# Kernel optimization log

Measured on AMD Instinct MI355X. Metric: run time of the kernel, lower is better.

## Reference

```python
import jax, jax.numpy as jnp
import numpy as np

D = 512      # model_dim
H = 8        # num_heads
HD = D // H  # head_dim = 64
S = 196      # tokens per channel (14x14 grid)
CHANNELS = np.array([2, 4, 6, 4], dtype=np.int32)  # multiplex channels per sample


def setup_inputs() -> dict:
    key = jax.random.key(0)
    ks = jax.random.split(key, 8)
    C = int(CHANNELS.sum())  # 16
    n = lambda k, shp, s=1.0: jax.random.normal(k, shp, dtype=jnp.float32) * s
    return {
        "x_query": n(ks[0], (C, S, D)),
        "x_keyval": n(ks[1], (C, S, D)),
        "pos": n(ks[2], (C, S, D)),
        "channels": CHANNELS,
        "Wq": n(ks[3], (D, D), 0.02), "bq": jnp.zeros((D,), jnp.float32),
        "Wk": n(ks[4], (D, D), 0.02), "bk": jnp.zeros((D,), jnp.float32),
        "Wv": n(ks[5], (D, D), 0.02), "bv": jnp.zeros((D,), jnp.float32),
        "Wo": n(ks[6], (D, D), 0.02), "bo": jnp.zeros((D,), jnp.float32),
    }


def reference(x_query, x_keyval, pos, channels, Wq, bq, Wk, bk, Wv, bv, Wo, bo):
    C, S_, D_ = x_query.shape
    ch = np.asarray(channels)
    # segment id per packed token; segment i has length channels[i]*S (== cu_seq_len blocks)
    seg = np.repeat(np.arange(ch.shape[0]), ch * S_)                # [T] static
    block_mask = seg[:, None] == seg[None, :]                        # [T,T] static bool

    xq = x_query.reshape(-1, D_)   # [T,D]
    xk = x_keyval.reshape(-1, D_)
    p = pos.reshape(-1, D_)

    # positional embedding fused into Q/K before projection (query_pos/key_pos)
    q = ((xq + p) @ Wq + bq).reshape(-1, H, HD)
    k = ((xk + p) @ Wk + bk).reshape(-1, H, HD)
    v = (xk @ Wv + bv).reshape(-1, H, HD)

    scale = 1.0 / np.sqrt(HD)
    scores = jnp.einsum('qhd,khd->hqk', q, k) * scale               # [H,T,T]
    scores = jnp.where(block_mask[None], scores, jnp.float32(-1e30))
    attn = jax.nn.softmax(scores, axis=-1)
    out = jnp.einsum('hqk,khd->qhd', attn, v).reshape(-1, D_)       # [T,D]
    out = out @ Wo + bo
    return out.reshape(C, S_, D_)
```

## Files before the change

kernel.cpp:

```cpp
#include <hip/hip_runtime.h>
#include <hip/hip_bf16.h>


typedef short short8 __attribute__((ext_vector_type(8)));
typedef float f32x4 __attribute__((ext_vector_type(4)));

__device__ __forceinline__ float b2f(unsigned short u) {
    union { float f; unsigned int i; } x; x.i = ((unsigned int)u) << 16; return x.f;
}
__device__ __forceinline__ unsigned short f2b(float f) {
    union { float f; unsigned int i; } x; x.f = f;
    unsigned int r = x.i + 0x7fffu + ((x.i >> 16) & 1u);
    return (unsigned short)(r >> 16);
}

#define NE 1605632
#define WE 262144
#define GS 72

__launch_bounds__(256)
__global__ void prep(const float* __restrict__ W0, const float* __restrict__ W1,
                     const float* __restrict__ W2, const float* __restrict__ W3,
                     unsigned short* __restrict__ WF) {
    const int tid = threadIdx.x;
    const float* W = blockIdx.z == 0 ? W0 : blockIdx.z == 1 ? W1 : blockIdx.z == 2 ? W2 : W3;
    unsigned short* T = WF + (size_t)blockIdx.z * WE;
    const int s = blockIdx.x * 4 + (tid >> 6);
    const int f = s >> 4, t = s & 15;
    const int lane = tid & 63, quad = lane >> 4, l16 = lane & 15;
    short8 o;
    #pragma unroll
    for (int j = 0; j < 8; ++j)
        o[j] = (short)f2b(W[(size_t)(t * 32 + quad * 8 + j) * 512 + f * 16 + l16]);
    *(short8*)(T + (size_t)s * 512 + lane * 8) = o;
}

__device__ __forceinline__ short8 castA(const float* __restrict__ X,
                                        const float* __restrict__ P, size_t off) {
    f32x4 x0 = *(const f32x4*)(X + off), x1 = *(const f32x4*)(X + off + 4);
    short8 r;
    if (P) {
        f32x4 p0 = *(const f32x4*)(P + off), p1 = *(const f32x4*)(P + off + 4);
        #pragma unroll
        for (int j = 0; j < 4; ++j) {
            r[j] = (short)f2b(x0[j] + p0[j]); r[4 + j] = (short)f2b(x1[j] + p1[j]);
        }
    } else {
        #pragma unroll
        for (int j = 0; j < 4; ++j) {
            r[j] = (short)f2b(x0[j]); r[4 + j] = (short)f2b(x1[j]);
        }
    }
    return r;
}

template <bool OUT_F32>
__device__ __forceinline__ void gemm_wave(const unsigned short* __restrict__ A,
                                          const unsigned short* __restrict__ WFw,
                                          const float* __restrict__ bias,
                                          void* __restrict__ C,
                                          int m0, int n0) {
    const int lane = threadIdx.x & 63;
    const int quad = lane >> 4, l16 = lane & 15;
    const int f0 = n0 >> 4;
    const unsigned short* Arow = A + (size_t)(m0 + l16) * 512 + quad * 8;
    const unsigned short* Bbase = WFw + (size_t)lane * 8;

    f32x4 acc[4] = {};
    #pragma unroll 4
    for (int t = 0; t < 16; ++t) {
        short8 af = *(const short8*)(Arow + t * 32);
        #pragma unroll
        for (int nt = 0; nt < 4; ++nt) {
            short8 bf = *(const short8*)(Bbase + (size_t)((f0 + nt) * 16 + t) * 512);
            acc[nt] = __builtin_amdgcn_mfma_f32_16x16x32_bf16(af, bf, acc[nt], 0, 0, 0);
        }
    }
    #pragma unroll
    for (int nt = 0; nt < 4; ++nt) {
        const int col = n0 + nt * 16 + l16;
        const float bv = bias[col];
        #pragma unroll
        for (int r = 0; r < 4; ++r) {
            const int row = m0 + quad * 4 + r;
            float cv = acc[nt][r] + bv;
            if constexpr (OUT_F32) ((float*)C)[(size_t)row * 512 + col] = cv;
            else ((unsigned short*)C)[(size_t)row * 512 + col] = f2b(cv);
        }
    }
}

__device__ __forceinline__ void gemm_wave32c(const float* __restrict__ X,
                                             const float* __restrict__ P,
                                             const unsigned short* __restrict__ WFw,
                                             const float* __restrict__ bias,
                                             unsigned short* __restrict__ C,
                                             int m0, int n0) {
    const int lane = threadIdx.x & 63;
    const int quad = lane >> 4, l16 = lane & 15;
    const int f0 = n0 >> 4;
    const size_t a0 = (size_t)(m0 + l16) * 512 + quad * 8;
    const unsigned short* Bbase = WFw + (size_t)lane * 8;

    f32x4 acc0[4] = {}, acc1[4] = {};
    #pragma unroll 4
    for (int t = 0; t < 16; ++t) {
        short8 af0 = castA(X, P, a0 + t * 32);
        short8 af1 = castA(X, P, a0 + 16 * 512 + t * 32);
        #pragma unroll
        for (int nt = 0; nt < 4; ++nt) {
            short8 bf = *(const short8*)(Bbase + (size_t)((f0 + nt) * 16 + t) * 512);
            acc0[nt] = __builtin_amdgcn_mfma_f32_16x16x32_bf16(af0, bf, acc0[nt], 0, 0, 0);
            acc1[nt] = __builtin_amdgcn_mfma_f32_16x16x32_bf16(af1, bf, acc1[nt], 0, 0, 0);
        }
    }
    #pragma unroll
    for (int nt = 0; nt < 4; ++nt) {
        const int col = n0 + nt * 16 + l16;
        const float bv = bias[col];
        #pragma unroll
        for (int r = 0; r < 4; ++r) {
            const int row = m0 + quad * 4 + r;
            C[(size_t)row * 512 + col]        = f2b(acc0[nt][r] + bv);
            C[(size_t)(row + 16) * 512 + col] = f2b(acc1[nt][r] + bv);
        }
    }
}

__launch_bounds__(256)
__global__ void qkv_gemm(const float* __restrict__ xq, const float* __restrict__ xk,
                         const float* __restrict__ pos,
                         const unsigned short* __restrict__ WF,
                         const float* __restrict__ bq, const float* __restrict__ bk,
                         const float* __restrict__ bv,
                         unsigned short* __restrict__ qb, unsigned short* __restrict__ kb,
                         unsigned short* __restrict__ vb) {
    const float* X; const float* P; const unsigned short* WFw; const float* bias;
    unsigned short* C;
    switch (blockIdx.z) {
        case 0:  X = xq; P = pos;     WFw = WF;          bias = bq; C = qb; break;
        case 1:  X = xk; P = pos;     WFw = WF + WE;     bias = bk; C = kb; break;
        default: X = xk; P = nullptr; WFw = WF + 2 * WE; bias = bv; C = vb; break;
    }
    const int w = threadIdx.x >> 6;
    gemm_wave32c(X, P, WFw, bias, C, blockIdx.x * 64 + (w & 1) * 32,
                 blockIdx.y * 128 + (w >> 1) * 64);
}

__launch_bounds__(256)
__global__ void out_gemm(const unsigned short* __restrict__ A,
                         const unsigned short* __restrict__ WFo,
                         const float* __restrict__ bo, float* __restrict__ out) {
    gemm_wave<true>(A, WFo, bo, out, blockIdx.x * 64 + (threadIdx.x >> 6) * 16,
                    blockIdx.y * 64);
}

__launch_bounds__(512)
__global__ void attn_seg(const unsigned short* __restrict__ q,
                         const unsigned short* __restrict__ k,
                         const unsigned short* __restrict__ v,
                         unsigned short* __restrict__ o) {
    __shared__ __align__(16) unsigned char Lds[55296];

    const int id = blockIdx.x;
    int h, off, L, qt;
    if (id < 152)      { h = id & 7; qt = id >> 3; off = 1176; L = 1176; }
    else if (id < 360) { int m = id - 152; h = m & 7; int s = m >> 3;
                         if (s < 13) { off = 392;  L = 784; qt = s; }
                         else        { off = 2352; L = 784; qt = s - 13; } }
    else               { int m = id - 360; h = m & 7; qt = m >> 3; off = 0; L = 392; }

    const int tid = threadIdx.x;
    const int wave = tid >> 6, lane = tid & 63;
    const int grp = wave >> 2, w4 = wave & 3;
    const int quad = lane >> 4, l16 = lane & 15;
    const int hb = h * 64;
    const int lastr = off + L - 1;

    unsigned short* Ks = (unsigned short*)(Lds + grp * 18432);
    unsigned short* Vt = (unsigned short*)(Lds + grp * 18432 + 9216);
    unsigned char*  Pme = Lds + 36864 + wave * 2304;

    int qrow = off + qt * 64 + w4 * 16 + l16;
    if (qrow > lastr) qrow = lastr;
    const short8 qf0 = *(const short8*)(q + (size_t)qrow * 512 + hb + quad * 8);
    const short8 qf1 = *(const short8*)(q + (size_t)qrow * 512 + hb + 32 + quad * 8);

    const int skey = lane, sd = w4 * 16;
    const int ntiles = (L + 63) >> 6;
    const int nt0 = (ntiles + 1) >> 1;

    float lsum = 0.f;
    f32x4 oacc[4] = {};

    short8 kr0, kr1, vr0, vr1;
    {
        int kk = (grp ? nt0 : 0) * 64 + skey;
        int krow = off + (kk < L ? kk : L - 1);
        kr0 = *(const short8*)(k + (size_t)krow * 512 + hb + sd);
        kr1 = *(const short8*)(k + (size_t)krow * 512 + hb + sd + 8);
        vr0 = *(const short8*)(v + (size_t)krow * 512 + hb + sd);
        vr1 = *(const short8*)(v + (size_t)krow * 512 + hb + sd + 8);
    }
    unsigned char* pwr = Pme + l16 * 144 + quad * 8;
    const unsigned char* prd = Pme + l16 * 144 + quad * 16;

    for (int i = 0; i < nt0; ++i) {
        const int tg = (grp ? nt0 : 0) + i;
        __syncthreads();
        *(short8*)(Ks + skey * GS + sd)     = kr0;
        *(short8*)(Ks + skey * GS + sd + 8) = kr1;
        #pragma unroll
        for (int j = 0; j < 8; ++j) {
            Vt[(sd + j) * GS + skey]     = (unsigned short)vr0[j];
            Vt[(sd + 8 + j) * GS + skey] = (unsigned short)vr1[j];
        }
        __syncthreads();
        if (i + 1 < nt0) {
            int kk = (tg + 1) * 64 + skey;
            int krow = off + (kk < L ? kk : L - 1);
            kr0 = *(const short8*)(k + (size_t)krow * 512 + hb + sd);
            kr1 = *(const short8*)(k + (size_t)krow * 512 + hb + sd + 8);
            vr0 = *(const short8*)(v + (size_t)krow * 512 + hb + sd);
            vr1 = *(const short8*)(v + (size_t)krow * 512 + hb + sd + 8);
        }
        f32x4 sT[4];
        #pragma unroll
        for (int g = 0; g < 4; ++g) {
            short8 kb0 = *(const short8*)(Ks + (g * 16 + l16) * GS + quad * 8);
            short8 kb1 = *(const short8*)(Ks + (g * 16 + l16) * GS + 32 + quad * 8);
            f32x4 z = {0.f, 0.f, 0.f, 0.f};
            z     = __builtin_amdgcn_mfma_f32_16x16x32_bf16(kb0, qf0, z, 0, 0, 0);
            sT[g] = __builtin_amdgcn_mfma_f32_16x16x32_bf16(kb1, qf1, z, 0, 0, 0);
        }
        const int kbase = tg * 64 + quad * 4;
        #pragma unroll
        for (int g = 0; g < 4; ++g) {
            float p[4];
            #pragma unroll
            for (int r = 0; r < 4; ++r) {
                const bool valid = (kbase + g * 16 + r) < L;
                p[r] = valid ? __expf(fminf(sT[g][r] * 0.125f, 30.f)) : 0.f;
                lsum += p[r];
            }
            #pragma unroll
            for (int i2 = 0; i2 < 2; ++i2) {
                __hip_bfloat162 t = __float22bfloat162_rn(make_float2(p[2 * i2], p[2 * i2 + 1]));
                *(unsigned int*)(pwr + g * 32 + i2 * 4) = *(unsigned int*)&t;
            }
        }
        short8 pa0 = *(const short8*)(prd);
        short8 pa1 = *(const short8*)(prd + 64);
        #pragma unroll
        for (int nt = 0; nt < 4; ++nt) {
            short8 vf0 = *(const short8*)(Vt + (nt * 16 + l16) * GS + quad * 8);
            short8 vf1 = *(const short8*)(Vt + (nt * 16 + l16) * GS + 32 + quad * 8);
            oacc[nt] = __builtin_amdgcn_mfma_f32_16x16x32_bf16(pa0, vf0, oacc[nt], 0, 0, 0);
            oacc[nt] = __builtin_amdgcn_mfma_f32_16x16x32_bf16(pa1, vf1, oacc[nt], 0, 0, 0);
        }
    }
    lsum += __shfl_xor(lsum, 16);
    lsum += __shfl_xor(lsum, 32);

    __syncthreads();
    float* Mrg = (float*)(Lds + w4 * 5120 + lane * 80);
    float* Ls  = (float*)(Lds + 20480);
    if (grp == 1) {
        #pragma unroll
        for (int nt = 0; nt < 4; ++nt) *(f32x4*)(Mrg + nt * 4) = oacc[nt];
        Ls[w4 * 64 + lane] = lsum;
    }
    __syncthreads();
    if (grp == 0) {
        lsum += Ls[w4 * 64 + lane];
        #pragma unroll
        for (int nt = 0; nt < 4; ++nt) {
            f32x4 po = *(const f32x4*)(Mrg + nt * 4);
            oacc[nt] += po;
        }
        #pragma unroll
        for (int r = 0; r < 4; ++r) {
            const float srow = __shfl(lsum, (lane & 48) + quad * 4 + r);
            const float linv = 1.0f / srow;
            const int qi = qt * 64 + w4 * 16 + quad * 4 + r;
            if (qi < L) {
                #pragma unroll
                for (int nt = 0; nt < 4; ++nt)
                    o[(size_t)(off + qi) * 512 + hb + nt * 16 + l16] = f2b(oacc[nt][r] * linv);
            }
        }
    }
}

extern "C" void kernel_launch(void* const* d_in, const int* in_sizes, int n_in,
                              void* d_out, int out_size, void* d_ws, size_t ws_size,
                              hipStream_t stream) {
    const float* xq  = (const float*)d_in[0];
    const float* xk  = (const float*)d_in[1];
    const float* pos = (const float*)d_in[2];
    const float* Wq = (const float*)d_in[4];
    const float* bq = (const float*)d_in[5];
    const float* Wk = (const float*)d_in[6];
    const float* bk = (const float*)d_in[7];
    const float* Wv = (const float*)d_in[8];
    const float* bv = (const float*)d_in[9];
    const float* Wo = (const float*)d_in[10];
    const float* bo = (const float*)d_in[11];
    float* out = (float*)d_out;

    unsigned short* ws = (unsigned short*)d_ws;
    unsigned short* qb = ws;
    unsigned short* kb = ws + NE;
    unsigned short* vb = ws + (size_t)2 * NE;
    unsigned short* WF = ws + (size_t)3 * NE;

    prep<<<dim3(128, 1, 4), 256, 0, stream>>>(Wq, Wk, Wv, Wo, WF);
    qkv_gemm<<<dim3(49, 4, 3), 256, 0, stream>>>(xq, xk, pos, WF, bq, bk, bv,
                                                 qb, kb, vb);
    attn_seg<<<dim3(416), 512, 0, stream>>>(qb, kb, vb, qb);
    out_gemm<<<dim3(49, 8), 256, 0, stream>>>(qb, WF + (size_t)3 * WE, bo, out);
}
```

Baseline: 165.5 us.

## Stage converted A tile in LDS and widen QKV GEMM to full N per block

```diff
diff --git a/kernel.cpp b/kernel.cpp
--- a/kernel.cpp
+++ b/kernel.cpp
@@ -5,9 +5,6 @@
 typedef short short8 __attribute__((ext_vector_type(8)));
 typedef float f32x4 __attribute__((ext_vector_type(4)));
 
-__device__ __forceinline__ float b2f(unsigned short u) {
-    union { float f; unsigned int i; } x; x.i = ((unsigned int)u) << 16; return x.f;
-}
 __device__ __forceinline__ unsigned short f2b(float f) {
     union { float f; unsigned int i; } x; x.f = f;
     unsigned int r = x.i + 0x7fffu + ((x.i >> 16) & 1u);
@@ -17,6 +14,7 @@
 #define NE 1605632
 #define WE 262144
 #define GS 72
+#define LDA 520
 
 __launch_bounds__(256)
 __global__ void prep(const float* __restrict__ W0, const float* __restrict__ W1,
@@ -35,98 +33,6 @@
     *(short8*)(T + (size_t)s * 512 + lane * 8) = o;
 }
 
-__device__ __forceinline__ short8 castA(const float* __restrict__ X,
-                                        const float* __restrict__ P, size_t off) {
-    f32x4 x0 = *(const f32x4*)(X + off), x1 = *(const f32x4*)(X + off + 4);
-    short8 r;
-    if (P) {
-        f32x4 p0 = *(const f32x4*)(P + off), p1 = *(const f32x4*)(P + off + 4);
-        #pragma unroll
-        for (int j = 0; j < 4; ++j) {
-            r[j] = (short)f2b(x0[j] + p0[j]); r[4 + j] = (short)f2b(x1[j] + p1[j]);
-        }
-    } else {
-        #pragma unroll
-        for (int j = 0; j < 4; ++j) {
-            r[j] = (short)f2b(x0[j]); r[4 + j] = (short)f2b(x1[j]);
-        }
-    }
-    return r;
-}
-
-template <bool OUT_F32>
-__device__ __forceinline__ void gemm_wave(const unsigned short* __restrict__ A,
-                                          const unsigned short* __restrict__ WFw,
-                                          const float* __restrict__ bias,
-                                          void* __restrict__ C,
-                                          int m0, int n0) {
-    const int lane = threadIdx.x & 63;
-    const int quad = lane >> 4, l16 = lane & 15;
-    const int f0 = n0 >> 4;
-    const unsigned short* Arow = A + (size_t)(m0 + l16) * 512 + quad * 8;
-    const unsigned short* Bbase = WFw + (size_t)lane * 8;
-
-    f32x4 acc[4] = {};
-    #pragma unroll 4
-    for (int t = 0; t < 16; ++t) {
-        short8 af = *(const short8*)(Arow + t * 32);
-        #pragma unroll
-        for (int nt = 0; nt < 4; ++nt) {
-            short8 bf = *(const short8*)(Bbase + (size_t)((f0 + nt) * 16 + t) * 512);
-            acc[nt] = __builtin_amdgcn_mfma_f32_16x16x32_bf16(af, bf, acc[nt], 0, 0, 0);
-        }
-    }
-    #pragma unroll
-    for (int nt = 0; nt < 4; ++nt) {
-        const int col = n0 + nt * 16 + l16;
-        const float bv = bias[col];
-        #pragma unroll
-        for (int r = 0; r < 4; ++r) {
-            const int row = m0 + quad * 4 + r;
-            float cv = acc[nt][r] + bv;
-            if constexpr (OUT_F32) ((float*)C)[(size_t)row * 512 + col] = cv;
-            else ((unsigned short*)C)[(size_t)row * 512 + col] = f2b(cv);
-        }
-    }
-}
-
-__device__ __forceinline__ void gemm_wave32c(const float* __restrict__ X,
-                                             const float* __restrict__ P,
-                                             const unsigned short* __restrict__ WFw,
-                                             const float* __restrict__ bias,
-                                             unsigned short* __restrict__ C,
-                                             int m0, int n0) {
-    const int lane = threadIdx.x & 63;
-    const int quad = lane >> 4, l16 = lane & 15;
-    const int f0 = n0 >> 4;
-    const size_t a0 = (size_t)(m0 + l16) * 512 + quad * 8;
-    const unsigned short* Bbase = WFw + (size_t)lane * 8;
-
-    f32x4 acc0[4] = {}, acc1[4] = {};
-    #pragma unroll 4
-    for (int t = 0; t < 16; ++t) {
-        short8 af0 = castA(X, P, a0 + t * 32);
-        short8 af1 = castA(X, P, a0 + 16 * 512 + t * 32);
-        #pragma unroll
-        for (int nt = 0; nt < 4; ++nt) {
-            short8 bf = *(const short8*)(Bbase + (size_t)((f0 + nt) * 16 + t) * 512);
-            acc0[nt] = __builtin_amdgcn_mfma_f32_16x16x32_bf16(af0, bf, acc0[nt], 0, 0, 0);
-            acc1[nt] = __builtin_amdgcn_mfma_f32_16x16x32_bf16(af1, bf, acc1[nt], 0, 0, 0);
-        }
-    }
-    #pragma unroll
-    for (int nt = 0; nt < 4; ++nt) {
-        const int col = n0 + nt * 16 + l16;
-        const float bv = bias[col];
-        #pragma unroll
-        for (int r = 0; r < 4; ++r) {
-            const int row = m0 + quad * 4 + r;
-            C[(size_t)row * 512 + col]        = f2b(acc0[nt][r] + bv);
-            C[(size_t)(row + 16) * 512 + col] = f2b(acc1[nt][r] + bv);
-        }
-    }
-}
-
 __launch_bounds__(256)
 __global__ void qkv_gemm(const float* __restrict__ xq, const float* __restrict__ xk,
                          const float* __restrict__ pos,
@@ -135,24 +41,111 @@
                          const float* __restrict__ bv,
                          unsigned short* __restrict__ qb, unsigned short* __restrict__ kb,
                          unsigned short* __restrict__ vb) {
-    const float* X; const float* P; const unsigned short* WFw; const float* bias;
-    unsigned short* C;
-    switch (blockIdx.z) {
-        case 0:  X = xq; P = pos;     WFw = WF;          bias = bq; C = qb; break;
-        case 1:  X = xk; P = pos;     WFw = WF + WE;     bias = bk; C = kb; break;
-        default: X = xk; P = nullptr; WFw = WF + 2 * WE; bias = bv; C = vb; break;
-    }
-    const int w = threadIdx.x >> 6;
-    gemm_wave32c(X, P, WFw, bias, C, blockIdx.x * 64 + (w & 1) * 32,
-                 blockIdx.y * 128 + (w >> 1) * 64);
+    __shared__ __align__(16) unsigned short As[32 * LDA];
+
+    const int z = blockIdx.z;
+    const float* X = (z == 0) ? xq : xk;
+    const bool addp = (z < 2);
+    const unsigned short* WFw = WF + (size_t)z * WE;
+    const float* bias = (z == 0) ? bq : (z == 1) ? bk : bv;
+    unsigned short* C = (z == 0) ? qb : (z == 1) ? kb : vb;
+
+    const int m0 = blockIdx.x * 32;
+    const int tid = threadIdx.x;
+
+    {
+        const int row = tid >> 3, ch = tid & 7;
+        const float* src = X + (size_t)(m0 + row) * 512 + ch * 64;
+        const float* ps  = pos + (size_t)(m0 + row) * 512 + ch * 64;
+        unsigned short* dst = As + row * LDA + ch * 64;
+        #pragma unroll
+        for (int i = 0; i < 8; ++i) {
+            f32x4 a = *(const f32x4*)(src + i * 8);
+            f32x4 b = *(const f32x4*)(src + i * 8 + 4);
+            if (addp) {
+                f32x4 pa = *(const f32x4*)(ps + i * 8);
+                f32x4 pb = *(const f32x4*)(ps + i * 8 + 4);
+                #pragma unroll
+                for (int j = 0; j < 4; ++j) { a[j] += pa[j]; b[j] += pb[j]; }
+            }
+            short8 o;
+            #pragma unroll
+            for (int j = 0; j < 4; ++j) {
+                o[j] = (short)f2b(a[j]); o[4 + j] = (short)f2b(b[j]);
+            }
+            *(short8*)(dst + i * 8) = o;
+        }
+    }
+    __syncthreads();
+
+    const int wave = tid >> 6, lane = tid & 63;
+    const int quad = lane >> 4, l16 = lane & 15;
+    const int rg = wave & 1, chf = wave >> 1;
+    const int n0 = chf * 256;
+    const unsigned short* Arow = As + (rg * 16 + l16) * LDA + quad * 8;
+    const unsigned short* Bbase = WFw + (size_t)lane * 8 + (size_t)n0 * 512;
+
+    f32x4 acc[16] = {};
+    #pragma unroll 4
+    for (int t = 0; t < 16; ++t) {
+        short8 af = *(const short8*)(Arow + t * 32);
+        #pragma unroll
+        for (int nt = 0; nt < 16; ++nt) {
+            short8 bf = *(const short8*)(Bbase + (size_t)(nt * 16 + t) * 512);
+            acc[nt] = __builtin_amdgcn_mfma_f32_16x16x32_bf16(af, bf, acc[nt], 0, 0, 0);
+        }
+    }
+    #pragma unroll
+    for (int nt = 0; nt < 16; ++nt) {
+        const int col = n0 + nt * 16 + l16;
+        const float bv2 = bias[col];
+        #pragma unroll
+        for (int r = 0; r < 4; ++r) {
+            const int row = m0 + rg * 16 + quad * 4 + r;
+            C[(size_t)row * 512 + col] = f2b(acc[nt][r] + bv2);
+        }
+    }
+}
+
+__device__ __forceinline__ void gemm_wave_f32(const unsigned short* __restrict__ A,
+                                              const unsigned short* __restrict__ WFw,
+                                              const float* __restrict__ bias,
+                                              float* __restrict__ C,
+                                              int m0, int n0) {
+    const int lane = threadIdx.x & 63;
+    const int quad = lane >> 4, l16 = lane & 15;
+    const int f0 = n0 >> 4;
+    const unsigned short* Arow = A + (size_t)(m0 + l16) * 512 + quad * 8;
+    const unsigned short* Bbase = WFw + (size_t)lane * 8;
+
+    f32x4 acc[4] = {};
+    #pragma unroll 4
+    for (int t = 0; t < 16; ++t) {
+        short8 af = *(const short8*)(Arow + t * 32);
+        #pragma unroll
+        for (int nt = 0; nt < 4; ++nt) {
+            short8 bf = *(const short8*)(Bbase + (size_t)((f0 + nt) * 16 + t) * 512);
+            acc[nt] = __builtin_amdgcn_mfma_f32_16x16x32_bf16(af, bf, acc[nt], 0, 0, 0);
+        }
+    }
+    #pragma unroll
+    for (int nt = 0; nt < 4; ++nt) {
+        const int col = n0 + nt * 16 + l16;
+        const float bv = bias[col];
+        #pragma unroll
+        for (int r = 0; r < 4; ++r) {
+            const int row = m0 + quad * 4 + r;
+            C[(size_t)row * 512 + col] = acc[nt][r] + bv;
+        }
+    }
 }
 
 __launch_bounds__(256)
 __global__ void out_gemm(const unsigned short* __restrict__ A,
                          const unsigned short* __restrict__ WFo,
                          const float* __restrict__ bo, float* __restrict__ out) {
-    gemm_wave<true>(A, WFo, bo, out, blockIdx.x * 64 + (threadIdx.x >> 6) * 16,
-                    blockIdx.y * 64);
+    gemm_wave_f32(A, WFo, bo, out, blockIdx.x * 64 + (threadIdx.x >> 6) * 16,
+                  blockIdx.y * 64);
 }
 
 __launch_bounds__(512)
@@ -315,7 +308,7 @@
     unsigned short* WF = ws + (size_t)3 * NE;
 
     prep<<<dim3(128, 1, 4), 256, 0, stream>>>(Wq, Wk, Wv, Wo, WF);
-    qkv_gemm<<<dim3(49, 4, 3), 256, 0, stream>>>(xq, xk, pos, WF, bq, bk, bv,
+    qkv_gemm<<<dim3(98, 1, 3), 256, 0, stream>>>(xq, xk, pos, WF, bq, bk, bv,
                                                  qb, kb, vb);
     attn_seg<<<dim3(416), 512, 0, stream>>>(qb, kb, vb, qb);
     out_gemm<<<dim3(49, 8), 256, 0, stream>>>(qb, WF + (size_t)3 * WE, bo, out);
```

After: 147.9 us. 1.12x faster.
